# Optimization experiments

Measured on AMD Instinct MI355X. Metric: run time of the kernel, lower is better.

## Reference

```python
import jax, jax.numpy as jnp
import numpy as np

D_MODEL = 1024
NUM_HEADS = 16
D_K = D_MODEL // NUM_HEADS
D_FF = 4096


def setup_inputs() -> dict:
    key = jax.random.key(0)
    ks = jax.random.split(key, 12)
    s = 1.0 / np.sqrt(D_MODEL)
    sf = 1.0 / np.sqrt(D_FF)
    return {
        "x": jax.random.normal(ks[0], (2, 2048, D_MODEL), dtype=jnp.float32),
        # nn.Linear weights are [out_features, in_features]
        "Wq": jax.random.uniform(ks[1], (D_MODEL, D_MODEL), jnp.float32, -s, s),
        "Wk": jax.random.uniform(ks[2], (D_MODEL, D_MODEL), jnp.float32, -s, s),
        "Wv": jax.random.uniform(ks[3], (D_MODEL, D_MODEL), jnp.float32, -s, s),
        "Wo": jax.random.uniform(ks[4], (D_MODEL, D_MODEL), jnp.float32, -s, s),
        "W1": jax.random.uniform(ks[5], (D_FF, D_MODEL), jnp.float32, -s, s),
        "W2": jax.random.uniform(ks[6], (D_MODEL, D_FF), jnp.float32, -sf, sf),
        "g1": jnp.ones((D_MODEL,), jnp.float32),
        "b1": jnp.zeros((D_MODEL,), jnp.float32),
        "g2": jnp.ones((D_MODEL,), jnp.float32),
        "b2": jnp.zeros((D_MODEL,), jnp.float32),
    }


def _layer_norm(x, gamma, beta, eps=1e-5):
    mu = jnp.mean(x, axis=-1, keepdims=True)
    var = jnp.mean((x - mu) ** 2, axis=-1, keepdims=True)
    return (x - mu) * jax.lax.rsqrt(var + eps) * gamma + beta


def reference(x, Wq, Wk, Wv, Wo, W1, W2, g1, b1, g2, b2):
    B, S, _ = x.shape
    H, Dk = NUM_HEADS, D_K
    # projections (Linear: x @ W.T), split heads -> [B, H, S, Dk]
    q = (x @ Wq.T).reshape(B, S, H, Dk).transpose(0, 2, 1, 3)
    k = (x @ Wk.T).reshape(B, S, H, Dk).transpose(0, 2, 1, 3)
    v = (x @ Wv.T).reshape(B, S, H, Dk).transpose(0, 2, 1, 3)
    scores = jnp.einsum('bhsd,bhtd->bhst', q, k) / jnp.sqrt(jnp.float32(Dk))
    attn = jax.nn.softmax(scores, axis=-1)
    out = jnp.einsum('bhst,bhtd->bhsd', attn, v)
    out = out.transpose(0, 2, 1, 3).reshape(B, S, H * Dk)
    out = out @ Wo.T
    x_after_attn = _layer_norm(x + out, g1, b1)
    ff = jax.nn.gelu(x_after_attn @ W1.T, approximate=False)
    ff_out = ff @ W2.T
    return _layer_norm(x_after_attn + ff_out, g2, b2)
```

## Files before the change

kernel.cpp:

```cpp
#include <hip/hip_runtime.h>
#include <hip/hip_bf16.h>
#include <cstdint>
#include <cstddef>

#define D_MODEL 1024
#define D_FF    4096
#define NTOK    4096
#define SEQ     2048
#define NH      16
#define DK      64
#define LDQ     3072

typedef __bf16 bf16;
typedef __bf16 bf16_8 __attribute__((ext_vector_type(8)));
typedef __bf16 bf16_4 __attribute__((ext_vector_type(4)));
typedef float  f32_4  __attribute__((ext_vector_type(4)));

__device__ __forceinline__ void async_copy16(const bf16* g, bf16* l) {
    __builtin_amdgcn_global_load_lds((const __attribute__((address_space(1))) void*)g,
                                     (__attribute__((address_space(3))) void*)l,
                                     16, 0, 0);
}

__global__ __launch_bounds__(256)
void cast_all(const float* __restrict__ x,  const float* __restrict__ Wq,
              const float* __restrict__ Wk, const float* __restrict__ Wv,
              const float* __restrict__ Wo, const float* __restrict__ W1,
              const float* __restrict__ W2,
              bf16* __restrict__ xb, bf16* __restrict__ Wqkvb,
              bf16* __restrict__ Wob, bf16* __restrict__ W1b,
              bf16* __restrict__ W2b) {
    const int blk = blockIdx.x;
    const float* s; bf16* d; int off;
    if (blk < 4096)       { s = x;  d = xb;              off = blk; }
    else if (blk < 5120)  { s = Wq; d = Wqkvb;           off = blk - 4096; }
    else if (blk < 6144)  { s = Wk; d = Wqkvb + 1048576; off = blk - 5120; }
    else if (blk < 7168)  { s = Wv; d = Wqkvb + 2097152; off = blk - 6144; }
    else if (blk < 8192)  { s = Wo; d = Wob;             off = blk - 7168; }
    else if (blk < 12288) { s = W1; d = W1b;             off = blk - 8192; }
    else                  { s = W2; d = W2b;             off = blk - 12288; }
    const int i = off * 1024 + threadIdx.x * 4;
    float4 v = *(const float4*)(s + i);
    bf16_4 o;
    o[0] = (bf16)v.x; o[1] = (bf16)v.y; o[2] = (bf16)v.z; o[3] = (bf16)v.w;
    *(bf16_4*)(d + i) = o;
}

template <int EPI>
__global__ __launch_bounds__(256, 2)
void gemm_bt(const bf16* __restrict__ A, const bf16* __restrict__ B,
             bf16* __restrict__ C0, size_t cstride, bf16* __restrict__ Vt,
             int M, int N, int ldk, int kLen) {
    __shared__ bf16 As[128 * 64];
    __shared__ bf16 Bs[128 * 64];
    const int tid  = threadIdx.x;
    const int wave = tid >> 6, lane = tid & 63;
    const int quad = lane >> 4, l15 = lane & 15;
    const int wm = wave >> 1, wn = wave & 1;
    const int bm = blockIdx.x, bn = blockIdx.y, z = blockIdx.z;

    const bf16* A0 = A + (size_t)bm * 128 * ldk + (size_t)z * kLen;
    const bf16* B0 = B + (size_t)bn * 128 * ldk + (size_t)z * kLen;

    f32_4 acc[4][4];
#pragma unroll
    for (int i = 0; i < 4; i++)
#pragma unroll
        for (int j = 0; j < 4; j++) acc[i][j] = (f32_4){0.f, 0.f, 0.f, 0.f};

    const int srow8 = lane >> 3;
    const int slog  = (lane & 7) ^ srow8;
    const int rx    = l15 & 7;

    for (int k0 = 0; k0 < kLen; k0 += 64) {
#pragma unroll
        for (int c = 0; c < 4; c++) {
            int row = c * 32 + wave * 8 + srow8;
            async_copy16(&A0[(size_t)row * ldk + k0 + slog * 8],
                         &As[(c * 32 + wave * 8) * 64]);
        }
#pragma unroll
        for (int c = 0; c < 4; c++) {
            int row = c * 32 + wave * 8 + srow8;
            async_copy16(&B0[(size_t)row * ldk + k0 + slog * 8],
                         &Bs[(c * 32 + wave * 8) * 64]);
        }
        __syncthreads();

#pragma unroll
        for (int kh = 0; kh < 2; kh++) {
            bf16_8 af[4], bfr[4];
#pragma unroll
            for (int mi = 0; mi < 4; mi++)
                af[mi] = *(const bf16_8*)&As[(wm * 64 + mi * 16 + l15) * 64 +
                                             (((kh * 4 + quad) ^ rx) * 8)];
#pragma unroll
            for (int ni = 0; ni < 4; ni++)
                bfr[ni] = *(const bf16_8*)&Bs[(wn * 64 + ni * 16 + l15) * 64 +
                                              (((kh * 4 + quad) ^ rx) * 8)];
#pragma unroll
            for (int mi = 0; mi < 4; mi++)
#pragma unroll
                for (int ni = 0; ni < 4; ni++)
                    acc[mi][ni] = __builtin_amdgcn_mfma_f32_16x16x32_bf16(
                        af[mi], bfr[ni], acc[mi][ni], 0, 0, 0);
        }
        __syncthreads();
    }

    bf16* C = C0 + (size_t)z * cstride;
    const int row0 = bm * 128 + wm * 64 + quad * 4;
    const int col0 = bn * 128 + wn * 64 + l15;

    if (EPI == 3 && bn >= 16) {
        const int bvt = bm >> 4;
#pragma unroll
        for (int mi = 0; mi < 4; mi++) {
            const int srow = (row0 + mi * 16) & 2047;
#pragma unroll
            for (int ni = 0; ni < 4; ni++) {
                const int ch = col0 + ni * 16 - 2048;
                bf16_4 w;
#pragma unroll
                for (int r = 0; r < 4; r++) w[r] = (bf16)acc[mi][ni][r];
                *(bf16_4*)&Vt[((size_t)(bvt * 1024 + ch)) * SEQ + srow] = w;
            }
        }
        return;
    }

#pragma unroll
    for (int mi = 0; mi < 4; mi++) {
#pragma unroll
        for (int ni = 0; ni < 4; ni++) {
#pragma unroll
            for (int r = 0; r < 4; r++) {
                int row = row0 + mi * 16 + r;
                int col = col0 + ni * 16;
                size_t idx = (size_t)row * N + col;
                float v = acc[mi][ni][r];
                if (EPI == 2) {
                    float g = 0.5f * v * (1.0f + erff(v * 0.70710678118654752f));
                    C[idx] = (bf16)g;
                } else {
                    C[idx] = (bf16)v;
                }
            }
        }
    }
}

__global__ __launch_bounds__(512)
void attn10(const bf16* __restrict__ QKV, const bf16* __restrict__ Vt,
            bf16* __restrict__ O) {
    __shared__ bf16 SM[2][8192];

    const int tid  = threadIdx.x;
    const int wave = tid >> 6, lane = tid & 63;
    const int quad = lane >> 4, l15 = lane & 15;
    const int qb = blockIdx.x & 15;
    const int h  = (blockIdx.x >> 4) & 15;
    const int b  = blockIdx.x >> 8;

    const bf16* Qg = QKV + (size_t)(b * SEQ) * LDQ + h * 64;
    const bf16* Kg = QKV + (size_t)(b * SEQ) * LDQ + 1024 + h * 64;
    const bf16* Vg = Vt + (size_t)(b * 1024 + h * 64) * SEQ;

    const int qrow = qb * 128 + wave * 16 + l15;
    const bf16_8 qf0 = *(const bf16_8*)&Qg[(size_t)qrow * LDQ + quad * 8];
    const bf16_8 qf1 = *(const bf16_8*)&Qg[(size_t)qrow * LDQ + 32 + quad * 8];

    const int m0 = wave * 8 + (lane >> 3);
    const int sg = lane & 7;
    const int sw = m0 & 7;
    const int xl = l15 & 7;
    const int fr = (((m0 >> 4) & 1) << 5) | ((m0 & 12) << 1) |
                   (((m0 >> 5) & 1) << 2) | (m0 & 3);

    bf16_8 one8;
#pragma unroll
    for (int i = 0; i < 8; i++) one8[i] = (bf16)1.0f;

    f32_4 lacc = (f32_4){0.f, 0.f, 0.f, 0.f};
    f32_4 o_acc[4];
#pragma unroll
    for (int d = 0; d < 4; d++) o_acc[d] = (f32_4){0.f, 0.f, 0.f, 0.f};

    async_copy16(&Kg[(size_t)fr * LDQ + ((sg ^ sw) * 8)],
                 &SM[0][wave * 512]);
    async_copy16(&Vg[(size_t)m0 * SEQ + ((sg ^ sw) * 8)],
                 &SM[0][4096 + wave * 512]);
    __syncthreads();

    for (int t = 0; t < SEQ / 64; ++t) {
        const int cur = t & 1;
        if (t + 1 < SEQ / 64) {
            const int k1 = (t + 1) * 64;
            async_copy16(&Kg[(size_t)(k1 + fr) * LDQ + ((sg ^ sw) * 8)],
                         &SM[cur ^ 1][wave * 512]);
            async_copy16(&Vg[(size_t)m0 * SEQ + k1 + ((sg ^ sw) * 8)],
                         &SM[cur ^ 1][4096 + wave * 512]);
        }

        const bf16* KsC = SM[cur];
        const bf16* VsC = SM[cur] + 4096;

        f32_4 s[4];
#pragma unroll
        for (int ni = 0; ni < 4; ni++) {
            const bf16* kp = &KsC[(ni * 16 + l15) * 64];
            bf16_8 kb0 = *(const bf16_8*)&kp[(quad ^ xl) * 8];
            bf16_8 kb1 = *(const bf16_8*)&kp[((quad + 4) ^ xl) * 8];
            f32_4 zz = (f32_4){0.f, 0.f, 0.f, 0.f};
            zz = __builtin_amdgcn_mfma_f32_16x16x32_bf16(kb0, qf0, zz, 0, 0, 0);
            s[ni] = __builtin_amdgcn_mfma_f32_16x16x32_bf16(kb1, qf1, zz, 0, 0, 0);
        }

        bf16_8 pf0, pf1;
#pragma unroll
        for (int ni = 0; ni < 4; ni++) {
#pragma unroll
            for (int r = 0; r < 4; r++) {
                float a = fmaf(s[ni][r], 0.18033688011112042f,
                               -11.541560327111708f);
                float p;
                asm("v_exp_f32 %0, %1" : "=v"(p) : "v"(a));
                bf16 pb = (bf16)p;
                const int jx = ((ni >> 1) << 2) + r;
                if ((ni & 1) == 0) pf0[jx] = pb;
                else               pf1[jx] = pb;
            }
        }

        lacc = __builtin_amdgcn_mfma_f32_16x16x32_bf16(one8, pf0, lacc, 0, 0, 0);
        lacc = __builtin_amdgcn_mfma_f32_16x16x32_bf16(one8, pf1, lacc, 0, 0, 0);

#pragma unroll
        for (int dt = 0; dt < 4; dt++) {
            const bf16* vp = &VsC[(dt * 16 + l15) * 64];
            bf16_8 vb0 = *(const bf16_8*)&vp[(quad ^ xl) * 8];
            bf16_8 vb1 = *(const bf16_8*)&vp[((quad + 4) ^ xl) * 8];
            o_acc[dt] = __builtin_amdgcn_mfma_f32_16x16x32_bf16(vb0, pf0, o_acc[dt], 0, 0, 0);
            o_acc[dt] = __builtin_amdgcn_mfma_f32_16x16x32_bf16(vb1, pf1, o_acc[dt], 0, 0, 0);
        }

        __syncthreads();
    }

    const float rl = 1.0f / lacc[0];

    bf16* P = (bf16*)SM + wave * 1280;
#pragma unroll
    for (int dt = 0; dt < 4; dt++) {
        bf16_4 pk;
#pragma unroll
        for (int r = 0; r < 4; r++) pk[r] = (bf16)(o_acc[dt][r] * rl);
        int G = dt * 2 + (quad >> 1);
        *(bf16_4*)&P[l15 * 80 + ((G ^ xl) * 8) + ((quad & 1) * 4)] = pk;
    }
    const int q2 = lane >> 2, dc = lane & 3, x2 = q2 & 7;
    bf16_8 o0 = *(const bf16_8*)&P[q2 * 80 + (((dc * 2) ^ x2) * 8)];
    bf16_8 o1 = *(const bf16_8*)&P[q2 * 80 + (((dc * 2 + 1) ^ x2) * 8)];
    const size_t row = (size_t)b * SEQ + qb * 128 + wave * 16 + q2;
    *(bf16_8*)&O[row * D_MODEL + h * 64 + dc * 16] = o0;
    *(bf16_8*)&O[row * D_MODEL + h * 64 + dc * 16 + 8] = o1;
}

template <bool A32, bool O32>
__global__ __launch_bounds__(256)
void ln_kernel(const void* __restrict__ av, const bf16* __restrict__ p0,
               const bf16* __restrict__ p1, const bf16* __restrict__ p2,
               const bf16* __restrict__ p3,
               const float* __restrict__ gamma, const float* __restrict__ beta,
               void* __restrict__ yv) {
    const int row = blockIdx.x;
    const int tid = threadIdx.x;
    const size_t off = (size_t)row * D_MODEL;
    float v[4];
    {
        bf16_4 a0 = *(const bf16_4*)(p0 + off + tid * 4);
        bf16_4 a1 = *(const bf16_4*)(p1 + off + tid * 4);
        bf16_4 a2 = *(const bf16_4*)(p2 + off + tid * 4);
        bf16_4 a3 = *(const bf16_4*)(p3 + off + tid * 4);
        if (A32) {
            float4 xa = *(const float4*)((const float*)av + off + tid * 4);
            v[0] = xa.x; v[1] = xa.y; v[2] = xa.z; v[3] = xa.w;
        } else {
            bf16_4 xa = *(const bf16_4*)((const bf16*)av + off + tid * 4);
#pragma unroll
            for (int i = 0; i < 4; i++) v[i] = (float)xa[i];
        }
#pragma unroll
        for (int i = 0; i < 4; i++)
            v[i] += ((float)a0[i] + (float)a1[i]) + ((float)a2[i] + (float)a3[i]);
    }
    float s = v[0] + v[1] + v[2] + v[3];
    float ss = v[0] * v[0] + v[1] * v[1] + v[2] * v[2] + v[3] * v[3];
#pragma unroll
    for (int m = 1; m < 64; m <<= 1) {
        s  += __shfl_xor(s, m);
        ss += __shfl_xor(ss, m);
    }
    __shared__ float red_s[4], red_q[4];
    int wave = tid >> 6, lane = tid & 63;
    if (lane == 0) { red_s[wave] = s; red_q[wave] = ss; }
    __syncthreads();
    s  = red_s[0] + red_s[1] + red_s[2] + red_s[3];
    ss = red_q[0] + red_q[1] + red_q[2] + red_q[3];
    float mu   = s * (1.f / D_MODEL);
    float var  = ss * (1.f / D_MODEL) - mu * mu;
    float rstd = rsqrtf(var + 1e-5f);
    float4 gg = *(const float4*)(gamma + tid * 4);
    float4 be = *(const float4*)(beta + tid * 4);
    float y0 = (v[0] - mu) * rstd * gg.x + be.x;
    float y1 = (v[1] - mu) * rstd * gg.y + be.y;
    float y2 = (v[2] - mu) * rstd * gg.z + be.z;
    float y3 = (v[3] - mu) * rstd * gg.w + be.w;
    if (O32) {
        *(float4*)((float*)yv + off + tid * 4) = make_float4(y0, y1, y2, y3);
    } else {
        bf16_4 o;
        o[0] = (bf16)y0; o[1] = (bf16)y1; o[2] = (bf16)y2; o[3] = (bf16)y3;
        *(bf16_4*)((bf16*)yv + off + tid * 4) = o;
    }
}

extern "C" void kernel_launch(void* const* d_in, const int* in_sizes, int n_in,
                              void* d_out, int out_size, void* d_ws, size_t ws_size,
                              hipStream_t stream) {
    (void)in_sizes; (void)n_in; (void)out_size; (void)ws_size;
    const float* x  = (const float*)d_in[0];
    const float* Wq = (const float*)d_in[1];
    const float* Wk = (const float*)d_in[2];
    const float* Wv = (const float*)d_in[3];
    const float* Wo = (const float*)d_in[4];
    const float* W1 = (const float*)d_in[5];
    const float* W2 = (const float*)d_in[6];
    const float* g1 = (const float*)d_in[7];
    const float* b1 = (const float*)d_in[8];
    const float* g2 = (const float*)d_in[9];
    const float* b2 = (const float*)d_in[10];

    char* ws = (char*)d_ws;
    bf16*  xb    = (bf16*)(ws + 0);
    bf16*  aob   = xb;
    bf16*  ln1b  = (bf16*)(ws + 0);
    bf16*  QKVb  = (bf16*)(ws + 8388608);
    bf16*  Vtb   = (bf16*)(ws + 33554432);
    bf16*  hb    = (bf16*)(ws + 8388608);
    bf16*  Wqkvb = (bf16*)(ws + 41943040);
    bf16*  Wob   = (bf16*)(ws + 48234496);
    bf16*  W1b   = (bf16*)(ws + 50331648);
    bf16*  W2b   = (bf16*)(ws + 58720256);
    bf16*  proj0 = (bf16*)(ws + 67108864);
    const size_t PSTRIDE = (size_t)NTOK * D_MODEL;

    cast_all<<<dim3(16384), 256, 0, stream>>>(x, Wq, Wk, Wv, Wo, W1, W2,
                                              xb, Wqkvb, Wob, W1b, W2b);

    gemm_bt<3><<<dim3(NTOK / 128, 3072 / 128, 1), 256, 0, stream>>>(
        xb, Wqkvb, QKVb, 0, Vtb, NTOK, 3072, D_MODEL, D_MODEL);

    attn10<<<dim3(512), 512, 0, stream>>>(QKVb, Vtb, aob);

    gemm_bt<0><<<dim3(NTOK / 128, D_MODEL / 128, 4), 256, 0, stream>>>(
        aob, Wob, proj0, PSTRIDE, nullptr, NTOK, D_MODEL, D_MODEL, 256);
    ln_kernel<true, false><<<NTOK, 256, 0, stream>>>(
        x, proj0, proj0 + PSTRIDE, proj0 + 2 * PSTRIDE, proj0 + 3 * PSTRIDE,
        g1, b1, ln1b);

    gemm_bt<2><<<dim3(NTOK / 128, D_FF / 128, 1), 256, 0, stream>>>(
        ln1b, W1b, hb, 0, nullptr, NTOK, D_FF, D_MODEL, D_MODEL);

    gemm_bt<0><<<dim3(NTOK / 128, D_MODEL / 128, 4), 256, 0, stream>>>(
        hb, W2b, proj0, PSTRIDE, nullptr, NTOK, D_MODEL, D_FF, 1024);
    ln_kernel<false, true><<<NTOK, 256, 0, stream>>>(
        ln1b, proj0, proj0 + PSTRIDE, proj0 + 2 * PSTRIDE, proj0 + 3 * PSTRIDE,
        g2, b2, d_out);
}
```

Baseline: 317.8 us.

## Add 128x256-tile triple-buffered GEMM kernel for FFN matmuls

Introduces a new GEMM kernel with 512-thread blocks, 128x256 output tiles, three-stage async LDS buffering and swizzled layout, and uses it for the two FFN matmuls (W1 with GELU epilogue, W2 split-K). The larger tile raises operand reuse per LDS load, and the deeper pipeline is meant to hide global memory latency better. It also removes the GELU branch from the original gemm_bt epilogue. The cost is more LDS per block (about 144KB) and fewer blocks in the grid, which may lower occupancy.

```diff
diff --git a/kernel.cpp b/kernel.cpp
--- a/kernel.cpp
+++ b/kernel.cpp
@@ -139,6 +139,108 @@
                 int col = col0 + ni * 16;
                 size_t idx = (size_t)row * N + col;
                 float v = acc[mi][ni][r];
+                C[idx] = (bf16)v;
+            }
+        }
+    }
+}
+
+template <int EPI>
+__global__ __launch_bounds__(512)
+void gemm2(const bf16* __restrict__ A, const bf16* __restrict__ B,
+           bf16* __restrict__ C0, size_t cstride,
+           int M, int N, int ldk, int kLen) {
+    __shared__ bf16 SA[3][128 * 64];
+    __shared__ bf16 SB[3][256 * 64];
+    const int tid  = threadIdx.x;
+    const int wave = tid >> 6, lane = tid & 63;
+    const int quad = lane >> 4, l15 = lane & 15;
+    const int wm = wave >> 2, wn = wave & 3;
+    const int bm = blockIdx.x, bn = blockIdx.y, z = blockIdx.z;
+
+    const bf16* A0 = A + (size_t)bm * 128 * ldk + (size_t)z * kLen;
+    const bf16* B0 = B + (size_t)bn * 256 * ldk + (size_t)z * kLen;
+
+    f32_4 acc[4][4];
+#pragma unroll
+    for (int i = 0; i < 4; i++)
+#pragma unroll
+        for (int j = 0; j < 4; j++) acc[i][j] = (f32_4){0.f, 0.f, 0.f, 0.f};
+
+    const int srow8 = lane >> 3;
+    const int slog  = (lane & 7) ^ srow8;
+    const int rx    = l15 & 7;
+
+    bf16* pA0 = SA[0]; bf16* pA1 = SA[1]; bf16* pA2 = SA[2];
+    bf16* pB0 = SB[0]; bf16* pB1 = SB[1]; bf16* pB2 = SB[2];
+
+    const int nt = kLen >> 6;
+
+#define STAGE2(As, Bs, k0)                                                    \
+    {                                                                         \
+        _Pragma("unroll")                                                     \
+        for (int c = 0; c < 2; c++) {                                         \
+            int row = c * 64 + wave * 8 + srow8;                              \
+            async_copy16(&A0[(size_t)row * ldk + (k0) + slog * 8],            \
+                         &(As)[(c * 64 + wave * 8) * 64]);                    \
+        }                                                                     \
+        _Pragma("unroll")                                                     \
+        for (int c = 0; c < 4; c++) {                                         \
+            int row = c * 64 + wave * 8 + srow8;                              \
+            async_copy16(&B0[(size_t)row * ldk + (k0) + slog * 8],            \
+                         &(Bs)[(c * 64 + wave * 8) * 64]);                    \
+        }                                                                     \
+    }
+
+    STAGE2(pA0, pB0, 0);
+    if (nt > 1) STAGE2(pA1, pB1, 64);
+
+    for (int t = 0; t < nt; ++t) {
+        if (t + 1 < nt) { asm volatile("s_waitcnt vmcnt(6)" ::: "memory"); }
+        else            { asm volatile("s_waitcnt vmcnt(0)" ::: "memory"); }
+        __builtin_amdgcn_s_barrier();
+        asm volatile("" ::: "memory");
+
+        if (t + 2 < nt) STAGE2(pA2, pB2, (t + 2) * 64);
+
+#pragma unroll
+        for (int kh = 0; kh < 2; kh++) {
+            bf16_8 af[4], bfr[4];
+#pragma unroll
+            for (int mi = 0; mi < 4; mi++)
+                af[mi] = *(const bf16_8*)&pA0[(wm * 64 + mi * 16 + l15) * 64 +
+                                              (((kh * 4 + quad) ^ rx) * 8)];
+#pragma unroll
+            for (int ni = 0; ni < 4; ni++)
+                bfr[ni] = *(const bf16_8*)&pB0[(wn * 64 + ni * 16 + l15) * 64 +
+                                               (((kh * 4 + quad) ^ rx) * 8)];
+#pragma unroll
+            for (int mi = 0; mi < 4; mi++)
+#pragma unroll
+                for (int ni = 0; ni < 4; ni++)
+                    acc[mi][ni] = __builtin_amdgcn_mfma_f32_16x16x32_bf16(
+                        af[mi], bfr[ni], acc[mi][ni], 0, 0, 0);
+        }
+
+        bf16* ta = pA0; pA0 = pA1; pA1 = pA2; pA2 = ta;
+        bf16* tb = pB0; pB0 = pB1; pB1 = pB2; pB2 = tb;
+    }
+#undef STAGE2
+
+    bf16* C = C0 + (size_t)z * cstride;
+    const int row0 = bm * 128 + wm * 64 + quad * 4;
+    const int col0 = bn * 256 + wn * 64 + l15;
+
+#pragma unroll
+    for (int mi = 0; mi < 4; mi++) {
+#pragma unroll
+        for (int ni = 0; ni < 4; ni++) {
+#pragma unroll
+            for (int r = 0; r < 4; r++) {
+                int row = row0 + mi * 16 + r;
+                int col = col0 + ni * 16;
+                size_t idx = (size_t)row * N + col;
+                float v = acc[mi][ni][r];
                 if (EPI == 2) {
                     float g = 0.5f * v * (1.0f + erff(v * 0.70710678118654752f));
                     C[idx] = (bf16)g;
@@ -369,11 +471,11 @@
         x, proj0, proj0 + PSTRIDE, proj0 + 2 * PSTRIDE, proj0 + 3 * PSTRIDE,
         g1, b1, ln1b);
 
-    gemm_bt<2><<<dim3(NTOK / 128, D_FF / 128, 1), 256, 0, stream>>>(
-        ln1b, W1b, hb, 0, nullptr, NTOK, D_FF, D_MODEL, D_MODEL);
-
-    gemm_bt<0><<<dim3(NTOK / 128, D_MODEL / 128, 4), 256, 0, stream>>>(
-        hb, W2b, proj0, PSTRIDE, nullptr, NTOK, D_MODEL, D_FF, 1024);
+    gemm2<2><<<dim3(NTOK / 128, D_FF / 256, 1), 512, 0, stream>>>(
+        ln1b, W1b, hb, 0, NTOK, D_FF, D_MODEL, D_MODEL);
+
+    gemm2<0><<<dim3(NTOK / 128, D_MODEL / 256, 4), 512, 0, stream>>>(
+        hb, W2b, proj0, PSTRIDE, NTOK, D_MODEL, D_FF, 1024);
     ln_kernel<false, true><<<NTOK, 256, 0, stream>>>(
         ln1b, proj0, proj0 + PSTRIDE, proj0 + 2 * PSTRIDE, proj0 + 3 * PSTRIDE,
         g2, b2, d_out);
```

Measured after the change: 334.6 us. 5.3% more time.

## Double-buffer LDS tiles in bf16 GEMM to overlap global loads with MFMA

Applied to the files above, without the earlier changes.

Converts the GEMM main loop from single-buffered shared-memory staging to a two-stage ping-pong pipeline. The next tile's async global-to-LDS copies are issued two iterations ahead, and vmcnt waits are used instead of a full sync, so loads overlap with MFMA compute. LDS use doubles to 64KB per block, which may limit the two-blocks-per-CU occupancy requested by launch bounds. The hand-written waitcnt counts must match the number of outstanding loads.

```diff
diff --git a/kernel.cpp b/kernel.cpp
--- a/kernel.cpp
+++ b/kernel.cpp
@@ -51,8 +51,8 @@
 void gemm_bt(const bf16* __restrict__ A, const bf16* __restrict__ B,
              bf16* __restrict__ C0, size_t cstride, bf16* __restrict__ Vt,
              int M, int N, int ldk, int kLen) {
-    __shared__ bf16 As[128 * 64];
-    __shared__ bf16 Bs[128 * 64];
+    __shared__ bf16 As[2][128 * 64];
+    __shared__ bf16 Bs[2][128 * 64];
     const int tid  = threadIdx.x;
     const int wave = tid >> 6, lane = tid & 63;
     const int quad = lane >> 4, l15 = lane & 15;
@@ -72,32 +72,46 @@
     const int slog  = (lane & 7) ^ srow8;
     const int rx    = l15 & 7;
 
-    for (int k0 = 0; k0 < kLen; k0 += 64) {
-#pragma unroll
-        for (int c = 0; c < 4; c++) {
-            int row = c * 32 + wave * 8 + srow8;
-            async_copy16(&A0[(size_t)row * ldk + k0 + slog * 8],
-                         &As[(c * 32 + wave * 8) * 64]);
-        }
-#pragma unroll
-        for (int c = 0; c < 4; c++) {
-            int row = c * 32 + wave * 8 + srow8;
-            async_copy16(&B0[(size_t)row * ldk + k0 + slog * 8],
-                         &Bs[(c * 32 + wave * 8) * 64]);
-        }
-        __syncthreads();
-
+    const int nt = kLen >> 6;
+
+#define STAGE_BT(buf, k0)                                                     \
+    {                                                                         \
+        _Pragma("unroll")                                                     \
+        for (int c = 0; c < 4; c++) {                                         \
+            int row = c * 32 + wave * 8 + srow8;                              \
+            async_copy16(&A0[(size_t)row * ldk + (k0) + slog * 8],            \
+                         &As[buf][(c * 32 + wave * 8) * 64]);                 \
+        }                                                                     \
+        _Pragma("unroll")                                                     \
+        for (int c = 0; c < 4; c++) {                                         \
+            int row = c * 32 + wave * 8 + srow8;                              \
+            async_copy16(&B0[(size_t)row * ldk + (k0) + slog * 8],            \
+                         &Bs[buf][(c * 32 + wave * 8) * 64]);                 \
+        }                                                                     \
+    }
+
+    STAGE_BT(0, 0);
+    if (nt > 1) STAGE_BT(1, 64);
+
+    for (int t = 0; t < nt; ++t) {
+        if (t + 1 < nt) { asm volatile("s_waitcnt vmcnt(8)" ::: "memory"); }
+        else            { asm volatile("s_waitcnt vmcnt(0)" ::: "memory"); }
+        __builtin_amdgcn_s_barrier();
+        asm volatile("" ::: "memory");
+
+        const bf16* Asc = As[t & 1];
+        const bf16* Bsc = Bs[t & 1];
 #pragma unroll
         for (int kh = 0; kh < 2; kh++) {
             bf16_8 af[4], bfr[4];
 #pragma unroll
             for (int mi = 0; mi < 4; mi++)
-                af[mi] = *(const bf16_8*)&As[(wm * 64 + mi * 16 + l15) * 64 +
-                                             (((kh * 4 + quad) ^ rx) * 8)];
+                af[mi] = *(const bf16_8*)&Asc[(wm * 64 + mi * 16 + l15) * 64 +
+                                              (((kh * 4 + quad) ^ rx) * 8)];
 #pragma unroll
             for (int ni = 0; ni < 4; ni++)
-                bfr[ni] = *(const bf16_8*)&Bs[(wn * 64 + ni * 16 + l15) * 64 +
-                                              (((kh * 4 + quad) ^ rx) * 8)];
+                bfr[ni] = *(const bf16_8*)&Bsc[(wn * 64 + ni * 16 + l15) * 64 +
+                                               (((kh * 4 + quad) ^ rx) * 8)];
 #pragma unroll
             for (int mi = 0; mi < 4; mi++)
 #pragma unroll
@@ -105,8 +119,13 @@
                     acc[mi][ni] = __builtin_amdgcn_mfma_f32_16x16x32_bf16(
                         af[mi], bfr[ni], acc[mi][ni], 0, 0, 0);
         }
-        __syncthreads();
-    }
+
+        asm volatile("" ::: "memory");
+        __builtin_amdgcn_s_barrier();
+
+        if (t + 2 < nt) STAGE_BT(t & 1, (t + 2) * 64);
+    }
+#undef STAGE_BT
 
     bf16* C = C0 + (size_t)z * cstride;
     const int row0 = bm * 128 + wm * 64 + quad * 4;
```

New measurement: 329.6 us. 1.04x slower.
